# Optimization experiments

Hardware: AMD Instinct MI355X
Metric: run time of the kernel (lower is better)

Reference implementation:

```python
import jax, jax.numpy as jnp
import numpy as np

N = 100000      # nodes
E = 1600000     # edges (without self loops)
G = 64          # graphs in batch
H = 4           # attention heads
C = 42          # hidden dim per head (node_hidden_dim)
DIN = 42        # node_input_dim
NEG_SLOPE = 0.2  # PyG GATConv default


def setup_inputs() -> dict:
    key = jax.random.key(0)
    ks = jax.random.split(key, 24)
    x = jax.random.normal(ks[0], (N, DIN), jnp.float32)
    # edges with src != dst (GATConv removes then re-adds self loops; we emulate
    # by generating loop-free edges and appending self loops in reference())
    src = jax.random.randint(ks[1], (E,), 0, N, dtype=jnp.int32)
    off = jax.random.randint(ks[2], (E,), 1, N, dtype=jnp.int32)
    dst = ((src + off) % N).astype(jnp.int32)
    edge_index = jnp.stack([src, dst])
    batch = jnp.sort(jax.random.randint(ks[3], (N,), 0, G, dtype=jnp.int32))
    s = 0.1
    inp = {
        'x': x, 'edge_index': edge_index, 'batch': batch,
        'lin0_w': s * jax.random.normal(ks[4], (DIN, C), jnp.float32),
        'lin0_b': jnp.zeros((C,), jnp.float32),
    }
    ins = [C, H * C, H * C]  # layer input widths: 42, 168, 168
    for l in range(3):
        inp[f'W{l+1}'] = s * jax.random.normal(ks[5 + 4 * l], (ins[l], H * C), jnp.float32)
        inp[f'asrc{l+1}'] = s * jax.random.normal(ks[6 + 4 * l], (H, C), jnp.float32)
        inp[f'adst{l+1}'] = s * jax.random.normal(ks[7 + 4 * l], (H, C), jnp.float32)
        inp[f'b{l+1}'] = jnp.zeros((H * C,), jnp.float32)
    return inp


def _gat_layer(x, src, dst, W, a_src, a_dst, bias):
    # x: [N, Fin] -> h: [N, H, C]
    h = (x @ W).reshape(N, H, C)
    alpha_src = jnp.sum(h * a_src[None], axis=-1)  # [N, H]
    alpha_dst = jnp.sum(h * a_dst[None], axis=-1)  # [N, H]
    e = jax.nn.leaky_relu(alpha_src[src] + alpha_dst[dst], NEG_SLOPE)  # [E', H]
    # segment softmax over incoming edges of each destination node
    m = jax.ops.segment_max(e, dst, num_segments=N)
    m = jnp.where(jnp.isfinite(m), m, 0.0)
    ex = jnp.exp(e - m[dst])
    denom = jax.ops.segment_sum(ex, dst, num_segments=N)
    alpha = ex / denom[dst]  # self loops guarantee denom > 0
    out = jax.ops.segment_sum(h[src] * alpha[:, :, None], dst, num_segments=N)
    return out.reshape(N, H * C) + bias


def reference(x, edge_index, batch, lin0_w, lin0_b,
              W1, asrc1, adst1, b1,
              W2, asrc2, adst2, b2,
              W3, asrc3, adst3, b3):
    x = jax.nn.elu(x @ lin0_w + lin0_b)
    loops = jnp.arange(N, dtype=edge_index.dtype)
    src = jnp.concatenate([edge_index[0], loops])
    dst = jnp.concatenate([edge_index[1], loops])
    for W, a_s, a_d, b in ((W1, asrc1, adst1, b1),
                           (W2, asrc2, adst2, b2),
                           (W3, asrc3, adst3, b3)):
        x = jax.nn.elu(_gat_layer(x, src, dst, W, a_s, a_d, b))
        # dropout p=0.0 -> identity; residual in original is computed but unused
    counts = jax.ops.segment_sum(jnp.ones((N,), x.dtype), batch, num_segments=G)
    sums = jax.ops.segment_sum(x, batch, num_segments=G)
    return sums / jnp.maximum(counts, 1.0)[:, None]  # [G, H*C]
```

## Files before the change

### kernel.cpp

```cpp
#include <hip/hip_runtime.h>
#include <hip/hip_fp16.h>
#include <cstdint>

#define HC 168
#define CC 42
#define NH 4
#define PH 44
#define HP 176
#define HPB 352
#define AP 192
#define A0P 64
#define NEG 0.2f

typedef _Float16 f16;
typedef __attribute__((ext_vector_type(8))) _Float16 f16x8;
typedef __attribute__((ext_vector_type(4))) float f32x4;

__device__ __forceinline__ float lrelu(float v) { return fmaxf(v, NEG * v); }
__device__ __forceinline__ float eluf(float v)  { return v > 0.f ? v : __expf(v) - 1.f; }

__device__ __forceinline__ float sel4(float4 w, int h) {
  float r = w.x;
  r = (h == 1) ? w.y : r;
  r = (h == 2) ? w.z : r;
  r = (h == 3) ? w.w : r;
  return r;
}

__global__ void cast16_kernel(const float* __restrict__ X, f16* __restrict__ O, int N) {
  int i = blockIdx.x * 256 + threadIdx.x;
  if (i >= N * A0P) return;
  int n = i >> 6, c = i & 63;
  O[i] = (c < CC) ? (f16)X[n * CC + c] : (f16)0.f;
}

__global__ void wconv_kernel(const float* __restrict__ W, f16* __restrict__ Wf,
                             int NCT, int KCN, int kpad, int Fink, int cpad, int Ncols,
                             int wstride) {
  int i = blockIdx.x * 256 + threadIdx.x;
  int tot = NCT * KCN * 64;
  if (i >= tot) return;
  int lane = i & 63;
  int t = i >> 6;
  int kc = t % KCN;
  int ct = t / KCN;
  int cl = ct * 16 + (lane & 15);
  int corig; bool cok;
  if (cpad) { int h = cl / PH, c = cl % PH; cok = (c < CC && h < NH); corig = h * CC + c; }
  else      { cok = (cl < Ncols); corig = cl; }
  f16 vals[8];
#pragma unroll
  for (int j = 0; j < 8; ++j) {
    int kp = kc * 32 + (lane >> 4) * 8 + j;
    int korig; bool kok;
    if (kpad) { int h = kp / PH, c = kp % PH; kok = (c < CC && h < NH && kp < HP); korig = h * CC + c; }
    else      { kok = (kp < Fink); korig = kp; }
    vals[j] = (kok && cok) ? (f16)W[korig * wstride + corig] : (f16)0.f;
  }
  *(f16x8*)(Wf + (size_t)i * 8) = *(f16x8*)vals;
}

__global__ __launch_bounds__(256) void mfma_gemm0_kernel(
    const f16* __restrict__ A, const f16* __restrict__ Wf,
    const float* __restrict__ bias, f16* __restrict__ Out, int N) {
  const int lane = threadIdx.x & 63;
  const int wid = (blockIdx.x * 256 + threadIdx.x) >> 6;
  const int row0 = wid * 16;
  if (row0 >= N) return;
  const int r = lane & 15, g = lane >> 4;
  f16x8 a[2];
  const f16* ap = A + (int64_t)(row0 + r) * A0P + g * 8;
#pragma unroll
  for (int kc = 0; kc < 2; ++kc) a[kc] = *(const f16x8*)(ap + kc * 32);
  f16* op = Out + (int64_t)row0 * A0P;
#pragma unroll
  for (int ct = 0; ct < 4; ++ct) {
    f32x4 acc = {0.f, 0.f, 0.f, 0.f};
#pragma unroll
    for (int kc = 0; kc < 2; ++kc) {
      f16x8 b = *(const f16x8*)(Wf + (((size_t)ct * 2 + kc) * 64 + lane) * 8);
      acc = __builtin_amdgcn_mfma_f32_16x16x32_f16(a[kc], b, acc, 0, 0, 0);
    }
    const int col = ct * 16 + r;
    float bv = (col < CC) ? bias[col] : 0.f;
#pragma unroll
    for (int v = 0; v < 4; ++v) {
      f16 o = (col < CC) ? (f16)eluf(acc[v] + bv) : (f16)0.f;
      op[(int64_t)(g * 4 + v) * A0P + col] = o;
    }
  }
}

template<int KCN>
__global__ __launch_bounds__(256) void mfma_gemmL_kernel(
    const f16* __restrict__ A, const f16* __restrict__ Wf,
    f16* __restrict__ Out, int N) {
  const int lane = threadIdx.x & 63;
  const int wid = (blockIdx.x * 256 + threadIdx.x) >> 6;
  const int row0 = wid * 16;
  if (row0 >= N) return;
  const int r = lane & 15, g = lane >> 4;
  f16x8 a[KCN];
  const f16* ap = A + (int64_t)(row0 + r) * (KCN * 32) + g * 8;
#pragma unroll
  for (int kc = 0; kc < KCN; ++kc) a[kc] = *(const f16x8*)(ap + kc * 32);
  f16* op = Out + (int64_t)row0 * HP;
#pragma unroll
  for (int ct = 0; ct < 11; ++ct) {
    f32x4 acc = {0.f, 0.f, 0.f, 0.f};
#pragma unroll
    for (int kc = 0; kc < KCN; ++kc) {
      f16x8 b = *(const f16x8*)(Wf + (((size_t)ct * KCN + kc) * 64 + lane) * 8);
      acc = __builtin_amdgcn_mfma_f32_16x16x32_f16(a[kc], b, acc, 0, 0, 0);
    }
    const int col = ct * 16 + r;
#pragma unroll
    for (int v = 0; v < 4; ++v)
      op[(int64_t)(g * 4 + v) * HP + col] = (f16)acc[v];
  }
}

__global__ void alpha_kernel(const __half2* __restrict__ H2,
                             const float* __restrict__ asrc,
                             const float* __restrict__ adst,
                             float* __restrict__ as_, float* __restrict__ ad_,
                             int N) {
  int i = blockIdx.x * 256 + threadIdx.x;
  if (i >= N * NH) return;
  int n = i >> 2, h = i & 3;
  const __half2* hp = H2 + (int64_t)n * (HP / 2) + h * (PH / 2);
  const float* ap = asrc + h * CC;
  const float* bp = adst + h * CC;
  float s = 0.f, d = 0.f;
#pragma unroll 7
  for (int j = 0; j < CC / 2; ++j) {
    float2 f = __half22float2(hp[j]);
    s += f.x * ap[2 * j] + f.y * ap[2 * j + 1];
    d += f.x * bp[2 * j] + f.y * bp[2 * j + 1];
  }
  as_[i] = s; ad_[i] = d;
}

__global__ void zero_i_kernel(int* __restrict__ p, int n) {
  int i = blockIdx.x * 256 + threadIdx.x;
  if (i < n) p[i] = 0;
}

__global__ void hist_kernel(const int* __restrict__ dst, int* __restrict__ cnt, int E) {
  int e = blockIdx.x * 256 + threadIdx.x;
  if (e < E) atomicAdd(&cnt[dst[e]], 1);
}

__global__ __launch_bounds__(256) void scan1_kernel(
    const int* __restrict__ cnt, int* __restrict__ rp1, int* __restrict__ blksum, int N) {
  __shared__ int lds[256];
  int t = threadIdx.x;
  int base = blockIdx.x * 1024 + t * 4;
  int v0 = (base + 0 < N) ? cnt[base + 0] : 0;
  int v1 = (base + 1 < N) ? cnt[base + 1] : 0;
  int v2 = (base + 2 < N) ? cnt[base + 2] : 0;
  int v3 = (base + 3 < N) ? cnt[base + 3] : 0;
  v1 += v0; v2 += v1; v3 += v2;
  lds[t] = v3;
  __syncthreads();
  for (int off = 1; off < 256; off <<= 1) {
    int add = (t >= off) ? lds[t - off] : 0;
    __syncthreads();
    lds[t] += add;
    __syncthreads();
  }
  int excl = lds[t] - v3;
  if (base + 0 < N) rp1[base + 0] = excl + v0;
  if (base + 1 < N) rp1[base + 1] = excl + v1;
  if (base + 2 < N) rp1[base + 2] = excl + v2;
  if (base + 3 < N) rp1[base + 3] = excl + v3;
  if (t == 255) blksum[blockIdx.x] = lds[255];
}

__global__ __launch_bounds__(256) void scan2_kernel(int* __restrict__ blksum, int nblk) {
  __shared__ int lds[256];
  int t = threadIdx.x;
  int v = (t < nblk) ? blksum[t] : 0;
  lds[t] = v;
  __syncthreads();
  for (int off = 1; off < 256; off <<= 1) {
    int add = (t >= off) ? lds[t - off] : 0;
    __syncthreads();
    lds[t] += add;
    __syncthreads();
  }
  if (t < nblk) blksum[t] = lds[t] - v;
}

__global__ void scan3_kernel(const int* __restrict__ blksum, int* __restrict__ rp1,
                             int* __restrict__ row_ptr0, int* __restrict__ cnt_cursor, int N) {
  int i = blockIdx.x * 256 + threadIdx.x;
  if (i >= N) return;
  int incl = rp1[i] + blksum[i >> 10];
  rp1[i] = incl;
  cnt_cursor[i] = incl - cnt_cursor[i];
  if (i == 0) row_ptr0[0] = 0;
}

__global__ void scatter_kernel(const int* __restrict__ src, const int* __restrict__ dst,
                               int* __restrict__ cursor, int* __restrict__ src_sorted, int E) {
  int e = blockIdx.x * 256 + threadIdx.x;
  if (e >= E) return;
  int pos = atomicAdd(&cursor[dst[e]], 1);
  src_sorted[pos] = src[e];
}

__global__ __launch_bounds__(256) void gat_agg_kernel(
    const int* __restrict__ row_ptr, const int* __restrict__ src_sorted,
    const f16* __restrict__ H16, const float4* __restrict__ as4,
    const float4* __restrict__ ad4_, const float* __restrict__ bias,
    f16* __restrict__ out, int N) {
  __shared__ int   loff[4][64];
  __shared__ float lw4[4][64][4];
  const int wv = threadIdx.x >> 6;
  const int lane = threadIdx.x & 63;
  const int wid = (blockIdx.x * 256 + threadIdx.x) >> 6;
  if (wid >= N) return;
  const int n = wid;
  const bool act = (lane < 44);
  const int hL = act ? (lane / 11) : 0;
  const int myoff = lane * 8;
  const float4 adn = ad4_[n];
  float ax = 0.f, ay = 0.f, az = 0.f, aw = 0.f, den = 0.f;

#define GAT_ACC(boff_, w_)                                                  \
  {                                                                         \
    den += w_;                                                              \
    if (act) {                                                              \
      float2 raw = *(const float2*)((const char*)H16 + (boff_) + myoff);    \
      __half2 u0 = *(__half2*)&raw.x, u1 = *(__half2*)&raw.y;               \
      float2 f0 = __half22float2(u0), f1 = __half22float2(u1);              \
      ax += f0.x * w_; ay += f0.y * w_;                                     \
      az += f1.x * w_; aw += f1.y * w_;                                     \
    }                                                                       \
  }

  {
    const float4 a4 = as4[n];
    float4 w4 = make_float4(__expf(lrelu(a4.x + adn.x)), __expf(lrelu(a4.y + adn.y)),
                            __expf(lrelu(a4.z + adn.z)), __expf(lrelu(a4.w + adn.w)));
    float w = sel4(w4, hL);
    GAT_ACC((int64_t)n * HPB, w);
  }

  const int beg = row_ptr[n], end = row_ptr[n + 1];
  for (int base = beg; base < end; base += 64) {
    const int m = min(64, end - base);
    int idx = (lane < m) ? src_sorted[base + lane] : n;
    float4 a4 = as4[idx];
    float4 w4 = make_float4(__expf(lrelu(a4.x + adn.x)), __expf(lrelu(a4.y + adn.y)),
                            __expf(lrelu(a4.z + adn.z)), __expf(lrelu(a4.w + adn.w)));
    loff[wv][lane] = idx * HPB;
    *(float4*)&lw4[wv][lane][0] = w4;

#define GAT_EDGE(jj)                                                        \
    {                                                                       \
      int boff = loff[wv][jj];                                              \
      float w = lw4[wv][jj][hL];                                            \
      GAT_ACC((int64_t)boff, w);                                            \
    }

    int j = 0;
    for (; j + 8 <= m; j += 8) {
      GAT_EDGE(j)     GAT_EDGE(j + 1) GAT_EDGE(j + 2) GAT_EDGE(j + 3)
      GAT_EDGE(j + 4) GAT_EDGE(j + 5) GAT_EDGE(j + 6) GAT_EDGE(j + 7)
    }
    for (; j < m; ++j) GAT_EDGE(j)
#undef GAT_EDGE
  }
#undef GAT_ACC

  if (lane < 48) {
    f16 o[4] = {(f16)0.f, (f16)0.f, (f16)0.f, (f16)0.f};
    if (act) {
      const int q = lane - hL * 11;
      const float acc[4] = {ax, ay, az, aw};
      const float rden = 1.f / den;
#pragma unroll
      for (int t = 0; t < 4; ++t) {
        int c = q * 4 + t;
        if (c < CC) o[t] = (f16)eluf(acc[t] * rden + bias[hL * CC + c]);
      }
    }
    *(uint2*)(out + (int64_t)n * AP + lane * 4) = *(uint2*)o;
  }
}

__global__ void gbound_kernel(const int* __restrict__ batch, int* __restrict__ gstart,
                              int N, int G) {
  int i = blockIdx.x * 256 + threadIdx.x;
  if (i > N) return;
  if (i == 0) {
    for (int g = 0; g <= batch[0]; ++g) gstart[g] = 0;
  } else if (i == N) {
    for (int g = batch[N - 1] + 1; g <= G; ++g) gstart[g] = N;
  } else {
    int a = batch[i - 1], b = batch[i];
    for (int g = a + 1; g <= b; ++g) gstart[g] = i;
  }
}

__global__ void zero_f_kernel(float* __restrict__ p, int n) {
  int i = blockIdx.x * 256 + threadIdx.x;
  if (i < n) p[i] = 0.f;
}

#define PSPLIT 4
__global__ __launch_bounds__(192) void pool2_kernel(
    const f16* __restrict__ x, const int* __restrict__ gstart,
    float* __restrict__ sums, int G) {
  int g = blockIdx.x;
  int t = threadIdx.x;
  if (t >= HC) return;
  int pos = (t / CC) * PH + t % CC;
  int beg = gstart[g], end = gstart[g + 1];
  float s = 0.f;
  for (int n = beg + (int)blockIdx.y; n < end; n += PSPLIT)
    s += (float)x[(int64_t)n * AP + pos];
  atomicAdd(sums + g * HC + t, s);
}

__global__ void out2_kernel(const float* __restrict__ sums, const int* __restrict__ gstart,
                            float* __restrict__ out, int G) {
  int i = blockIdx.x * 256 + threadIdx.x;
  if (i >= G * HC) return;
  int g = i / HC;
  float cnt = (float)(gstart[g + 1] - gstart[g]);
  out[i] = sums[i] / fmaxf(cnt, 1.f);
}

static inline int cdiv(int64_t a, int b) { return (int)((a + b - 1) / b); }

extern "C" void kernel_launch(void* const* d_in, const int* in_sizes, int n_in,
                              void* d_out, int out_size, void* d_ws, size_t ws_size,
                              hipStream_t stream) {
  const float* x      = (const float*)d_in[0];
  const int*   eidx   = (const int*)d_in[1];
  const int*   batch  = (const int*)d_in[2];
  const float* lin0_w = (const float*)d_in[3];
  const float* lin0_b = (const float*)d_in[4];
  const float* W[3]  = {(const float*)d_in[5],  (const float*)d_in[9],  (const float*)d_in[13]};
  const float* As[3] = {(const float*)d_in[6],  (const float*)d_in[10], (const float*)d_in[14]};
  const float* Ad[3] = {(const float*)d_in[7],  (const float*)d_in[11], (const float*)d_in[15]};
  const float* Bi[3] = {(const float*)d_in[8],  (const float*)d_in[12], (const float*)d_in[16]};

  const int N = in_sizes[2];
  const int E = in_sizes[1] / 2;
  const int G = out_size / HC;
  const int* src = eidx;
  const int* dst = eidx + E;

  char* p = (char*)d_ws;
  f16* x16  = (f16*)p;  p += (size_t)N * A0P * 2;
  f16* act0 = (f16*)p;  p += (size_t)N * A0P * 2;
  f16* actv = (f16*)p;  p += (size_t)N * AP * 2;
  f16* h16  = (f16*)p;  p += (size_t)N * HP * 2;
  f16* Wf0  = (f16*)p;  p += (size_t)4 * 2 * 64 * 8 * 2;
  f16* Wf1  = (f16*)p;  p += (size_t)11 * 2 * 64 * 8 * 2;
  f16* Wf2  = (f16*)p;  p += (size_t)11 * 6 * 64 * 8 * 2;
  f16* Wf3  = (f16*)p;  p += (size_t)11 * 6 * 64 * 8 * 2;
  float* as_  = (float*)p; p += (size_t)N * NH * 4;
  float* ad_  = (float*)p; p += (size_t)N * NH * 4;
  float* sums = (float*)p; p += (size_t)G * HC * 4;
  int* gstart     = (int*)p; p += (size_t)(G + 1) * 4;
  int* row_ptr    = (int*)p; p += (size_t)(N + 1) * 4;
  int* cursor     = (int*)p; p += (size_t)N * 4;
  int* blksum     = (int*)p; p += 256 * 4;
  int* src_sorted = (int*)p; p += (size_t)E * 4;
  (void)ws_size;

  const int nblk = cdiv(N, 1024);
  const int mfma_blocks = cdiv(cdiv(N, 16), 4);

  cast16_kernel<<<cdiv((int64_t)N * A0P, 256), 256, 0, stream>>>(x, x16, N);
  wconv_kernel<<<cdiv(4 * 2 * 64, 256),  256, 0, stream>>>(lin0_w, Wf0, 4, 2, 0, CC, 0, CC, CC);
  wconv_kernel<<<cdiv(11 * 2 * 64, 256), 256, 0, stream>>>(W[0], Wf1, 11, 2, 0, CC, 1, HC, HC);
  wconv_kernel<<<cdiv(11 * 6 * 64, 256), 256, 0, stream>>>(W[1], Wf2, 11, 6, 1, HC, 1, HC, HC);
  wconv_kernel<<<cdiv(11 * 6 * 64, 256), 256, 0, stream>>>(W[2], Wf3, 11, 6, 1, HC, 1, HC, HC);

  mfma_gemm0_kernel<<<mfma_blocks, 256, 0, stream>>>(x16, Wf0, lin0_b, act0, N);

  zero_i_kernel<<<cdiv(N, 256), 256, 0, stream>>>(cursor, N);
  hist_kernel<<<cdiv(E, 256), 256, 0, stream>>>(dst, cursor, E);
  scan1_kernel<<<nblk, 256, 0, stream>>>(cursor, row_ptr + 1, blksum, N);
  scan2_kernel<<<1, 256, 0, stream>>>(blksum, nblk);
  scan3_kernel<<<cdiv(N, 256), 256, 0, stream>>>(blksum, row_ptr + 1, row_ptr, cursor, N);
  scatter_kernel<<<cdiv(E, 256), 256, 0, stream>>>(src, dst, cursor, src_sorted, E);

  gbound_kernel<<<cdiv(N + 1, 256), 256, 0, stream>>>(batch, gstart, N, G);

  for (int l = 0; l < 3; ++l) {
    if (l == 0)
      mfma_gemmL_kernel<2><<<mfma_blocks, 256, 0, stream>>>(act0, Wf1, h16, N);
    else
      mfma_gemmL_kernel<6><<<mfma_blocks, 256, 0, stream>>>(actv, (l == 1) ? Wf2 : Wf3, h16, N);
    alpha_kernel<<<cdiv((int64_t)N * NH, 256), 256, 0, stream>>>(
        (const __half2*)h16, As[l], Ad[l], as_, ad_, N);
    gat_agg_kernel<<<cdiv(N, 4), 256, 0, stream>>>(
        row_ptr, src_sorted, h16, (const float4*)as_, (const float4*)ad_, Bi[l], actv, N);
  }

  zero_f_kernel<<<cdiv(G * HC, 256), 256, 0, stream>>>(sums, G * HC);
  pool2_kernel<<<dim3(G, PSPLIT), 192, 0, stream>>>(actv, gstart, sums, G);
  out2_kernel<<<cdiv(G * HC, 256), 256, 0, stream>>>(sums, gstart, (float*)d_out, G);
}
```

Before: 887.6 us.

## Fuse attention-score dot products into GEMM epilogue and merge small prep kernels

Computes alpha_src/alpha_dst inside the per-layer MFMA GEMM epilogue using padded attention vectors and wave shuffles, which removes the separate alpha kernel and its re-read of h. It also folds the fp32-to-fp16 input cast into the first GEMM's A-load, merges the weight conversions and buffer zeroing into one prep kernel, and fuses graph-boundary computation into the scatter kernel. Together these cut kernel launches and an extra pass over the node features. In exchange the GEMM epilogue carries more registers and shuffle work, and the first GEMM now does unvectorized fp32 loads.

```diff
diff --git a/kernel.cpp b/kernel.cpp
--- a/kernel.cpp
+++ b/kernel.cpp
@@ -27,19 +27,9 @@
   return r;
 }
 
-__global__ void cast16_kernel(const float* __restrict__ X, f16* __restrict__ O, int N) {
-  int i = blockIdx.x * 256 + threadIdx.x;
-  if (i >= N * A0P) return;
-  int n = i >> 6, c = i & 63;
-  O[i] = (c < CC) ? (f16)X[n * CC + c] : (f16)0.f;
-}
-
-__global__ void wconv_kernel(const float* __restrict__ W, f16* __restrict__ Wf,
-                             int NCT, int KCN, int kpad, int Fink, int cpad, int Ncols,
-                             int wstride) {
-  int i = blockIdx.x * 256 + threadIdx.x;
-  int tot = NCT * KCN * 64;
-  if (i >= tot) return;
+__device__ __forceinline__ void wconv_item(
+    const float* __restrict__ W, f16* __restrict__ Wf, int i,
+    int KCN, int kpad, int Fink, int cpad, int Ncols, int wstride) {
   int lane = i & 63;
   int t = i >> 6;
   int kc = t % KCN;
@@ -60,8 +50,42 @@
   *(f16x8*)(Wf + (size_t)i * 8) = *(f16x8*)vals;
 }
 
+__global__ void prep_kernel(
+    const float* __restrict__ lin0_w,
+    const float* __restrict__ W1, const float* __restrict__ W2, const float* __restrict__ W3,
+    const float* __restrict__ as1, const float* __restrict__ ad1,
+    const float* __restrict__ as2, const float* __restrict__ ad2,
+    const float* __restrict__ as3, const float* __restrict__ ad3,
+    f16* __restrict__ Wf0, f16* __restrict__ Wf1, f16* __restrict__ Wf2, f16* __restrict__ Wf3,
+    float* __restrict__ aPad,
+    int* __restrict__ cursor, float* __restrict__ sums,
+    int N, int G) {
+  const int W0N = 4 * 2 * 64, W1N = 11 * 2 * 64, W2N = 11 * 6 * 64;
+  int i = blockIdx.x * 256 + threadIdx.x;
+  if (i < N) { cursor[i] = 0; return; }
+  i -= N;
+  if (i < G * HC) { sums[i] = 0.f; return; }
+  i -= G * HC;
+  if (i < 3 * 2 * 176) {
+    int l = i / 352, rem = i % 352, which = rem / 176, col = rem % 176;
+    const float* tabs[6] = {as1, ad1, as2, ad2, as3, ad3};
+    const float* tab = tabs[l * 2 + which];
+    int h = col / PH, c = col % PH;
+    aPad[i] = (c < CC) ? tab[h * CC + c] : 0.f;
+    return;
+  }
+  i -= 3 * 2 * 176;
+  if (i < W0N) { wconv_item(lin0_w, Wf0, i, 2, 0, CC, 0, CC, CC); return; }
+  i -= W0N;
+  if (i < W1N) { wconv_item(W1, Wf1, i, 2, 0, CC, 1, HC, HC); return; }
+  i -= W1N;
+  if (i < W2N) { wconv_item(W2, Wf2, i, 6, 1, HC, 1, HC, HC); return; }
+  i -= W2N;
+  if (i < W2N) { wconv_item(W3, Wf3, i, 6, 1, HC, 1, HC, HC); return; }
+}
+
 __global__ __launch_bounds__(256) void mfma_gemm0_kernel(
-    const f16* __restrict__ A, const f16* __restrict__ Wf,
+    const float* __restrict__ X, const f16* __restrict__ Wf,
     const float* __restrict__ bias, f16* __restrict__ Out, int N) {
   const int lane = threadIdx.x & 63;
   const int wid = (blockIdx.x * 256 + threadIdx.x) >> 6;
@@ -69,9 +93,15 @@
   if (row0 >= N) return;
   const int r = lane & 15, g = lane >> 4;
   f16x8 a[2];
-  const f16* ap = A + (int64_t)(row0 + r) * A0P + g * 8;
-#pragma unroll
-  for (int kc = 0; kc < 2; ++kc) a[kc] = *(const f16x8*)(ap + kc * 32);
+  const float* xp = X + (int64_t)(row0 + r) * CC;
+#pragma unroll
+  for (int kc = 0; kc < 2; ++kc) {
+#pragma unroll
+    for (int j = 0; j < 8; ++j) {
+      int k = kc * 32 + g * 8 + j;
+      a[kc][j] = (k < CC) ? (f16)xp[k] : (f16)0.f;
+    }
+  }
   f16* op = Out + (int64_t)row0 * A0P;
 #pragma unroll
   for (int ct = 0; ct < 4; ++ct) {
@@ -94,7 +124,9 @@
 template<int KCN>
 __global__ __launch_bounds__(256) void mfma_gemmL_kernel(
     const f16* __restrict__ A, const f16* __restrict__ Wf,
-    f16* __restrict__ Out, int N) {
+    const float* __restrict__ asP, const float* __restrict__ adP,
+    f16* __restrict__ Out, float4* __restrict__ as4, float4* __restrict__ ad4,
+    int N) {
   const int lane = threadIdx.x & 63;
   const int wid = (blockIdx.x * 256 + threadIdx.x) >> 6;
   const int row0 = wid * 16;
@@ -105,6 +137,12 @@
 #pragma unroll
   for (int kc = 0; kc < KCN; ++kc) a[kc] = *(const f16x8*)(ap + kc * 32);
   f16* op = Out + (int64_t)row0 * HP;
+  float psA[4][4], psD[4][4];
+#pragma unroll
+  for (int h = 0; h < 4; ++h)
+#pragma unroll
+    for (int v = 0; v < 4; ++v) { psA[h][v] = 0.f; psD[h][v] = 0.f; }
+
 #pragma unroll
   for (int ct = 0; ct < 11; ++ct) {
     f32x4 acc = {0.f, 0.f, 0.f, 0.f};
@@ -114,36 +152,43 @@
       acc = __builtin_amdgcn_mfma_f32_16x16x32_f16(a[kc], b, acc, 0, 0, 0);
     }
     const int col = ct * 16 + r;
-#pragma unroll
-    for (int v = 0; v < 4; ++v)
-      op[(int64_t)(g * 4 + v) * HP + col] = (f16)acc[v];
-  }
-}
-
-__global__ void alpha_kernel(const __half2* __restrict__ H2,
-                             const float* __restrict__ asrc,
-                             const float* __restrict__ adst,
-                             float* __restrict__ as_, float* __restrict__ ad_,
-                             int N) {
-  int i = blockIdx.x * 256 + threadIdx.x;
-  if (i >= N * NH) return;
-  int n = i >> 2, h = i & 3;
-  const __half2* hp = H2 + (int64_t)n * (HP / 2) + h * (PH / 2);
-  const float* ap = asrc + h * CC;
-  const float* bp = adst + h * CC;
-  float s = 0.f, d = 0.f;
-#pragma unroll 7
-  for (int j = 0; j < CC / 2; ++j) {
-    float2 f = __half22float2(hp[j]);
-    s += f.x * ap[2 * j] + f.y * ap[2 * j + 1];
-    d += f.x * bp[2 * j] + f.y * bp[2 * j + 1];
-  }
-  as_[i] = s; ad_[i] = d;
-}
-
-__global__ void zero_i_kernel(int* __restrict__ p, int n) {
-  int i = blockIdx.x * 256 + threadIdx.x;
-  if (i < n) p[i] = 0;
+    const float aS = asP[col], aD = adP[col];
+    const int hlo = (ct * 16) / PH;
+    const bool hi = (col >= (hlo + 1) * PH);
+#pragma unroll
+    for (int v = 0; v < 4; ++v) {
+      f16 hq = (f16)acc[v];
+      op[(int64_t)(g * 4 + v) * HP + col] = hq;
+      float hf = (float)hq;
+      float tA = hf * aS, tD = hf * aD;
+      psA[hlo][v] += hi ? 0.f : tA;
+      psD[hlo][v] += hi ? 0.f : tD;
+      if (hlo < 3) {
+        psA[hlo + 1][v] += hi ? tA : 0.f;
+        psD[hlo + 1][v] += hi ? tD : 0.f;
+      }
+    }
+  }
+#pragma unroll
+  for (int h = 0; h < 4; ++h)
+#pragma unroll
+    for (int v = 0; v < 4; ++v) {
+      float aa = psA[h][v], dd = psD[h][v];
+#pragma unroll
+      for (int m = 1; m < 16; m <<= 1) {
+        aa += __shfl_xor(aa, m, 64);
+        dd += __shfl_xor(dd, m, 64);
+      }
+      psA[h][v] = aa; psD[h][v] = dd;
+    }
+  if (r < 4) {
+    int row = row0 + g * 4 + r;
+    as4[row] = make_float4(psA[0][r], psA[1][r], psA[2][r], psA[3][r]);
+  } else if (r < 8) {
+    int rr = r - 4;
+    int row = row0 + g * 4 + rr;
+    ad4[row] = make_float4(psD[0][rr], psD[1][rr], psD[2][rr], psD[3][rr]);
+  }
 }
 
 __global__ void hist_kernel(const int* __restrict__ dst, int* __restrict__ cnt, int E) {
@@ -202,12 +247,26 @@
   if (i == 0) row_ptr0[0] = 0;
 }
 
-__global__ void scatter_kernel(const int* __restrict__ src, const int* __restrict__ dst,
-                               int* __restrict__ cursor, int* __restrict__ src_sorted, int E) {
-  int e = blockIdx.x * 256 + threadIdx.x;
-  if (e >= E) return;
-  int pos = atomicAdd(&cursor[dst[e]], 1);
-  src_sorted[pos] = src[e];
+__global__ void scatter_gbound_kernel(
+    const int* __restrict__ src, const int* __restrict__ dst,
+    int* __restrict__ cursor, int* __restrict__ src_sorted,
+    const int* __restrict__ batch, int* __restrict__ gstart,
+    int E, int N, int G) {
+  int i = blockIdx.x * 256 + threadIdx.x;
+  if (i <= N) {
+    if (i == 0) {
+      for (int g = 0; g <= batch[0]; ++g) gstart[g] = 0;
+    } else if (i == N) {
+      for (int g = batch[N - 1] + 1; g <= G; ++g) gstart[g] = N;
+    } else {
+      int a = batch[i - 1], b = batch[i];
+      for (int g = a + 1; g <= b; ++g) gstart[g] = i;
+    }
+  }
+  if (i < E) {
+    int pos = atomicAdd(&cursor[dst[i]], 1);
+    src_sorted[pos] = src[i];
+  }
 }
 
 __global__ __launch_bounds__(256) void gat_agg_kernel(
@@ -291,25 +350,6 @@
   }
 }
 
-__global__ void gbound_kernel(const int* __restrict__ batch, int* __restrict__ gstart,
-                              int N, int G) {
-  int i = blockIdx.x * 256 + threadIdx.x;
-  if (i > N) return;
-  if (i == 0) {
-    for (int g = 0; g <= batch[0]; ++g) gstart[g] = 0;
-  } else if (i == N) {
-    for (int g = batch[N - 1] + 1; g <= G; ++g) gstart[g] = N;
-  } else {
-    int a = batch[i - 1], b = batch[i];
-    for (int g = a + 1; g <= b; ++g) gstart[g] = i;
-  }
-}
-
-__global__ void zero_f_kernel(float* __restrict__ p, int n) {
-  int i = blockIdx.x * 256 + threadIdx.x;
-  if (i < n) p[i] = 0.f;
-}
-
 #define PSPLIT 4
 __global__ __launch_bounds__(192) void pool2_kernel(
     const f16* __restrict__ x, const int* __restrict__ gstart,
@@ -356,7 +396,6 @@
   const int* dst = eidx + E;
 
   char* p = (char*)d_ws;
-  f16* x16  = (f16*)p;  p += (size_t)N * A0P * 2;
   f16* act0 = (f16*)p;  p += (size_t)N * A0P * 2;
   f16* actv = (f16*)p;  p += (size_t)N * AP * 2;
   f16* h16  = (f16*)p;  p += (size_t)N * HP * 2;
@@ -364,6 +403,7 @@
   f16* Wf1  = (f16*)p;  p += (size_t)11 * 2 * 64 * 8 * 2;
   f16* Wf2  = (f16*)p;  p += (size_t)11 * 6 * 64 * 8 * 2;
   f16* Wf3  = (f16*)p;  p += (size_t)11 * 6 * 64 * 8 * 2;
+  float* aPad = (float*)p; p += (size_t)3 * 2 * 176 * 4;
   float* as_  = (float*)p; p += (size_t)N * NH * 4;
   float* ad_  = (float*)p; p += (size_t)N * NH * 4;
   float* sums = (float*)p; p += (size_t)G * HC * 4;
@@ -377,35 +417,35 @@
   const int nblk = cdiv(N, 1024);
   const int mfma_blocks = cdiv(cdiv(N, 16), 4);
 
-  cast16_kernel<<<cdiv((int64_t)N * A0P, 256), 256, 0, stream>>>(x, x16, N);
-  wconv_kernel<<<cdiv(4 * 2 * 64, 256),  256, 0, stream>>>(lin0_w, Wf0, 4, 2, 0, CC, 0, CC, CC);
-  wconv_kernel<<<cdiv(11 * 2 * 64, 256), 256, 0, stream>>>(W[0], Wf1, 11, 2, 0, CC, 1, HC, HC);
-  wconv_kernel<<<cdiv(11 * 6 * 64, 256), 256, 0, stream>>>(W[1], Wf2, 11, 6, 1, HC, 1, HC, HC);
-  wconv_kernel<<<cdiv(11 * 6 * 64, 256), 256, 0, stream>>>(W[2], Wf3, 11, 6, 1, HC, 1, HC, HC);
-
-  mfma_gemm0_kernel<<<mfma_blocks, 256, 0, stream>>>(x16, Wf0, lin0_b, act0, N);
-
-  zero_i_kernel<<<cdiv(N, 256), 256, 0, stream>>>(cursor, N);
+  {
+    int tot = N + G * HC + 3 * 2 * 176 + 4 * 2 * 64 + 11 * 2 * 64 + 2 * (11 * 6 * 64);
+    prep_kernel<<<cdiv(tot, 256), 256, 0, stream>>>(
+        lin0_w, W[0], W[1], W[2], As[0], Ad[0], As[1], Ad[1], As[2], Ad[2],
+        Wf0, Wf1, Wf2, Wf3, aPad, cursor, sums, N, G);
+  }
+
+  mfma_gemm0_kernel<<<mfma_blocks, 256, 0, stream>>>(x, Wf0, lin0_b, act0, N);
+
   hist_kernel<<<cdiv(E, 256), 256, 0, stream>>>(dst, cursor, E);
   scan1_kernel<<<nblk, 256, 0, stream>>>(cursor, row_ptr + 1, blksum, N);
   scan2_kernel<<<1, 256, 0, stream>>>(blksum, nblk);
   scan3_kernel<<<cdiv(N, 256), 256, 0, stream>>>(blksum, row_ptr + 1, row_ptr, cursor, N);
-  scatter_kernel<<<cdiv(E, 256), 256, 0, stream>>>(src, dst, cursor, src_sorted, E);
-
-  gbound_kernel<<<cdiv(N + 1, 256), 256, 0, stream>>>(batch, gstart, N, G);
+  scatter_gbound_kernel<<<cdiv(E > N + 1 ? E : N + 1, 256), 256, 0, stream>>>(
+      src, dst, cursor, src_sorted, batch, gstart, E, N, G);
 
   for (int l = 0; l < 3; ++l) {
+    const float* asP = aPad + l * 352;
+    const float* adP = aPad + l * 352 + 176;
     if (l == 0)
-      mfma_gemmL_kernel<2><<<mfma_blocks, 256, 0, stream>>>(act0, Wf1, h16, N);
+      mfma_gemmL_kernel<2><<<mfma_blocks, 256, 0, stream>>>(
+          act0, Wf1, asP, adP, h16, (float4*)as_, (float4*)ad_, N);
     else
-      mfma_gemmL_kernel<6><<<mfma_blocks, 256, 0, stream>>>(actv, (l == 1) ? Wf2 : Wf3, h16, N);
-    alpha_kernel<<<cdiv((int64_t)N * NH, 256), 256, 0, stream>>>(
-        (const __half2*)h16, As[l], Ad[l], as_, ad_, N);
+      mfma_gemmL_kernel<6><<<mfma_blocks, 256, 0, stream>>>(
+          actv, (l == 1) ? Wf2 : Wf3, asP, adP, h16, (float4*)as_, (float4*)ad_, N);
     gat_agg_kernel<<<cdiv(N, 4), 256, 0, stream>>>(
         row_ptr, src_sorted, h16, (const float4*)as_, (const float4*)ad_, Bi[l], actv, N);
   }
 
-  zero_f_kernel<<<cdiv(G * HC, 256), 256, 0, stream>>>(sums, G * HC);
   pool2_kernel<<<dim3(G, PSPLIT), 192, 0, stream>>>(actv, gstart, sums, G);
   out2_kernel<<<cdiv(G * HC, 256), 256, 0, stream>>>(sums, gstart, (float*)d_out, G);
 }
```

Result: no change. 894.2 us (+0.7%).
